# Kernel tuning notes

Measured on AMD Instinct MI355X. Metric: run time of the kernel, lower is better.

The kernel has to match this reference:

```python
import jax, jax.numpy as jnp
import numpy as np

RADIUS = 1
WIN = 2 * RADIUS + 1


def setup_inputs() -> dict:
    key = jax.random.key(0)
    k1, k2 = jax.random.split(key)
    shape = (2, 64, 80, 80, 80)  # (b, c, d, h, w)
    x = jax.random.normal(k1, shape, dtype=jnp.float32)
    y = jax.random.normal(k2, shape, dtype=jnp.float32)
    return {"x": x, "y": y}


def reference(x, y):
    b, c, d, h, w = x.shape
    # zero-pad y by RADIUS on all three spatial dims
    y_padded = jnp.pad(
        y, ((0, 0), (0, 0), (RADIUS, RADIUS), (RADIUS, RADIUS), (RADIUS, RADIUS))
    )
    corrs = []
    for dz in range(WIN):
        for dy in range(WIN):
            for dx in range(WIN):
                y_win = y_padded[:, :, dz:dz + d, dy:dy + h, dx:dx + w]
                # channel-summed correlation for this offset -> [b, d, h, w]
                corrs.append(jnp.sum(x * y_win, axis=1))
    corr = jnp.stack(corrs, axis=1)
    return corr * (c ** -0.5)
```

## Files before the change

kernel.cpp:

```cpp
#include <hip/hip_runtime.h>

#define NT 320
#define TZ 4
#define TH 4
#define PZ 6
#define PH 6
#define STR 84
#define PROWS (PZ*PH)
#define NSLOT (PROWS*20)

__device__ __forceinline__ void store_f4u(float* p, float4 v) {
    __builtin_memcpy(p, &v, 16);
}

__global__ __launch_bounds__(NT)
void wincorr_kernel(const float* __restrict__ x, const float* __restrict__ y,
                    float* __restrict__ out)
{
    __shared__ __align__(16) float buf[2][PROWS * STR];

    const long long plane = 512000;
    const int tid = threadIdx.x;
    const int twi = tid % 20;
    const int th  = (tid / 20) % TH;
    const int tz  = tid / 80;

    const int zt = blockIdx.x, ht = blockIdx.y, b = blockIdx.z;
    const int z0 = zt * TZ, h0 = ht * TH;
    const int gz = z0 + tz, gh = h0 + th, wb = 4 * twi;

    const float* xb = x + (long long)b * 64 * plane;
    const float* yb = y + (long long)b * 64 * plane;
    const long long xoff = (long long)gz * 6400 + gh * 80 + wb;
    const long long xoffm = xoff - (wb > 0 ? 1 : 0);
    const long long xoffp = xoff + (wb < 76 ? 4 : 3);

    int  goff[3], loff[3];
    bool val[3];
    const bool inr2 = (tid + 2 * NT) < NSLOT;
#pragma unroll
    for (int k = 0; k < 3; ++k) {
        int s   = tid + k * NT;
        int row = s / 20, col = s % 20;
        int pz = row / PH, py = row % PH;
        int yz = z0 - 1 + pz, yh = h0 - 1 + py;
        bool ok = (s < NSLOT) && ((unsigned)yz < 80u) && ((unsigned)yh < 80u);
        val[k]  = ok;
        goff[k] = yz * 6400 + yh * 80 + 4 * col;
        loff[k] = row * STR + 4 * col;
    }

    float4 acc[27];
#pragma unroll
    for (int o = 0; o < 27; ++o) acc[o] = make_float4(0.f, 0.f, 0.f, 0.f);

    const float4 zero4 = make_float4(0.f, 0.f, 0.f, 0.f);
    float4 v0, v1, v2;

    {
        const float* yc = yb;
        v0 = val[0] ? *(const float4*)(yc + goff[0]) : zero4;
        v1 = val[1] ? *(const float4*)(yc + goff[1]) : zero4;
        v2 = val[2] ? *(const float4*)(yc + goff[2]) : zero4;
        *(float4*)(&buf[0][loff[0]]) = v0;
        *(float4*)(&buf[0][loff[1]]) = v1;
        if (inr2) *(float4*)(&buf[0][loff[2]]) = v2;
    }
    __syncthreads();

    for (int c = 0; c < 64; ++c) {
        const float* xcp = xb + (long long)c * plane;
        const float4 xv  = *(const float4*)(xcp + xoff);
        const float  xml = xcp[xoffm];
        const float  xpr = xcp[xoffp];

        if (c < 63) {
            const float* yc = yb + (long long)(c + 1) * plane;
            v0 = val[0] ? *(const float4*)(yc + goff[0]) : zero4;
            v1 = val[1] ? *(const float4*)(yc + goff[1]) : zero4;
            v2 = val[2] ? *(const float4*)(yc + goff[2]) : zero4;
        }

        const float* B = buf[c & 1];
#pragma unroll
        for (int dz = 0; dz < 3; ++dz) {
#pragma unroll
            for (int dy = 0; dy < 3; ++dy) {
                const float4 r = *(const float4*)(B + ((tz + dz) * PH + (th + dy)) * STR + wb);
                const int o = (dz * 3 + dy) * 3;
                acc[o].x   += xv.y * r.x; acc[o].y   += xv.z * r.y;
                acc[o].z   += xv.w * r.z; acc[o].w   += xpr  * r.w;
                acc[o+1].x += xv.x * r.x; acc[o+1].y += xv.y * r.y;
                acc[o+1].z += xv.z * r.z; acc[o+1].w += xv.w * r.w;
                acc[o+2].x += xml  * r.x; acc[o+2].y += xv.x * r.y;
                acc[o+2].z += xv.y * r.z; acc[o+2].w += xv.z * r.w;
            }
        }

        if (c < 63) {
            float* W = (float*)buf[(c + 1) & 1];
            *(float4*)(W + loff[0]) = v0;
            *(float4*)(W + loff[1]) = v1;
            if (inr2) *(float4*)(W + loff[2]) = v2;
        }
        __syncthreads();
    }

    float* ob = out + (long long)b * 27 * plane + xoff;
#pragma unroll
    for (int dz = 0; dz < 3; ++dz) {
#pragma unroll
        for (int dy = 0; dy < 3; ++dy) {
            const int o = (dz * 3 + dy) * 3;
            float4 a0 = acc[o], a1 = acc[o+1], a2 = acc[o+2];
            a0.x *= 0.125f; a0.y *= 0.125f; a0.z *= 0.125f; a0.w *= 0.125f;
            a1.x *= 0.125f; a1.y *= 0.125f; a1.z *= 0.125f; a1.w *= 0.125f;
            a2.x *= 0.125f; a2.y *= 0.125f; a2.z *= 0.125f; a2.w *= 0.125f;
            float* p0 = ob + (long long)(o    ) * plane;
            float* p1 = ob + (long long)(o + 1) * plane;
            float* p2 = ob + (long long)(o + 2) * plane;
            if (twi < 19) store_f4u(p0 + 1, a0);
            else { p0[1] = a0.x; p0[2] = a0.y; p0[3] = a0.z; }
            if (twi == 0) p0[0] = 0.f;
            *(float4*)p1 = a1;
            if (twi > 0) store_f4u(p2 - 1, a2);
            else { p2[0] = a2.y; p2[1] = a2.z; p2[2] = a2.w; }
            if (twi == 19) p2[3] = 0.f;
        }
    }
}

extern "C" void kernel_launch(void* const* d_in, const int* in_sizes, int n_in,
                              void* d_out, int out_size, void* d_ws, size_t ws_size,
                              hipStream_t stream) {
    const float* x = (const float*)d_in[0];
    const float* y = (const float*)d_in[1];
    float* out = (float*)d_out;

    dim3 grid(80 / TZ, 80 / TH, 2);
    dim3 block(NT);
    wincorr_kernel<<<grid, block, 0, stream>>>(x, y, out);
}
```

Before: 709.6 us.

## Deepen channel prefetch pipeline to two stages and cap registers for occupancy

```diff
diff --git a/kernel.cpp b/kernel.cpp
--- a/kernel.cpp
+++ b/kernel.cpp
@@ -13,7 +13,7 @@
     __builtin_memcpy(p, &v, 16);
 }
 
-__global__ __launch_bounds__(NT)
+__global__ __launch_bounds__(NT, 3)
 void wincorr_kernel(const float* __restrict__ x, const float* __restrict__ y,
                     float* __restrict__ out)
 {
@@ -55,33 +55,53 @@
     for (int o = 0; o < 27; ++o) acc[o] = make_float4(0.f, 0.f, 0.f, 0.f);
 
     const float4 zero4 = make_float4(0.f, 0.f, 0.f, 0.f);
-    float4 v0, v1, v2;
 
     {
         const float* yc = yb;
-        v0 = val[0] ? *(const float4*)(yc + goff[0]) : zero4;
-        v1 = val[1] ? *(const float4*)(yc + goff[1]) : zero4;
-        v2 = val[2] ? *(const float4*)(yc + goff[2]) : zero4;
-        *(float4*)(&buf[0][loff[0]]) = v0;
-        *(float4*)(&buf[0][loff[1]]) = v1;
-        if (inr2) *(float4*)(&buf[0][loff[2]]) = v2;
+        float4 t0 = val[0] ? *(const float4*)(yc + goff[0]) : zero4;
+        float4 t1 = val[1] ? *(const float4*)(yc + goff[1]) : zero4;
+        float4 t2 = val[2] ? *(const float4*)(yc + goff[2]) : zero4;
+        *(float4*)(&buf[0][loff[0]]) = t0;
+        *(float4*)(&buf[0][loff[1]]) = t1;
+        if (inr2) *(float4*)(&buf[0][loff[2]]) = t2;
     }
+    float4 yA0, yA1, yA2, yB0 = zero4, yB1 = zero4, yB2 = zero4;
+    {
+        const float* yc = yb + plane;
+        yA0 = val[0] ? *(const float4*)(yc + goff[0]) : zero4;
+        yA1 = val[1] ? *(const float4*)(yc + goff[1]) : zero4;
+        yA2 = val[2] ? *(const float4*)(yc + goff[2]) : zero4;
+    }
+    float4 xvA = *(const float4*)(xb + xoff);
+    float  xmA = xb[xoffm];
+    float  xpA = xb[xoffp];
+    float4 xvB = zero4; float xmB = 0.f, xpB = 0.f;
+
     __syncthreads();
 
+#pragma unroll 2
     for (int c = 0; c < 64; ++c) {
-        const float* xcp = xb + (long long)c * plane;
-        const float4 xv  = *(const float4*)(xcp + xoff);
-        const float  xml = xcp[xoffm];
-        const float  xpr = xcp[xoffp];
-
         if (c < 63) {
-            const float* yc = yb + (long long)(c + 1) * plane;
-            v0 = val[0] ? *(const float4*)(yc + goff[0]) : zero4;
-            v1 = val[1] ? *(const float4*)(yc + goff[1]) : zero4;
-            v2 = val[2] ? *(const float4*)(yc + goff[2]) : zero4;
+            float* W = (float*)buf[(c + 1) & 1];
+            *(float4*)(W + loff[0]) = yA0;
+            *(float4*)(W + loff[1]) = yA1;
+            if (inr2) *(float4*)(W + loff[2]) = yA2;
+        }
+        if (c < 62) {
+            const float* yc = yb + (long long)(c + 2) * plane;
+            yB0 = val[0] ? *(const float4*)(yc + goff[0]) : zero4;
+            yB1 = val[1] ? *(const float4*)(yc + goff[1]) : zero4;
+            yB2 = val[2] ? *(const float4*)(yc + goff[2]) : zero4;
+        }
+        if (c < 63) {
+            const float* xcp = xb + (long long)(c + 1) * plane;
+            xvB = *(const float4*)(xcp + xoff);
+            xmB = xcp[xoffm];
+            xpB = xcp[xoffp];
         }
 
         const float* B = buf[c & 1];
+        const float4 xv = xvA; const float xml = xmA, xpr = xpA;
 #pragma unroll
         for (int dz = 0; dz < 3; ++dz) {
 #pragma unroll
@@ -97,13 +117,9 @@
             }
         }
 
-        if (c < 63) {
-            float* W = (float*)buf[(c + 1) & 1];
-            *(float4*)(W + loff[0]) = v0;
-            *(float4*)(W + loff[1]) = v1;
-            if (inr2) *(float4*)(W + loff[2]) = v2;
-        }
         __syncthreads();
+        xvA = xvB; xmA = xmB; xpA = xpB;
+        yA0 = yB0; yA1 = yB1; yA2 = yB2;
     }
 
     float* ob = out + (long long)b * 27 * plane + xoff;
```

New measurement: 1.364 ms. 1.92x slower.
